# Optimization experiments

Measured on AMD Instinct MI355X. Metric: run time of the kernel, lower is better.

Reference implementation:

```python
import jax, jax.numpy as jnp
import numpy as np

SNUM = 8           # number of select-PUF stages
PUF_LEN = 64       # arbiter PUF length -> phi dim = PUF_LEN + 1
BATCH = 262144     # number of challenge-response pairs
D = 2 ** SNUM      # 256 combinations


def _make_kron_tables():
    """Replicates the W/B kron construction from combineMPUF.__init__.
    Returns Wmat, Bmat of shape [SNUM, D]; row i is W[i]/B[i] (originally [1, D])."""
    tmpX = np.array([[1], [1]])
    Ws, Bs = [], []
    for i in range(SNUM):
        w = np.array([[-1], [1]])
        b = np.array([[1], [0]])
        for _ in range(i + 1, SNUM):
            w = np.kron(tmpX, w)
            b = np.kron(tmpX, b)
        for _ in range(i):
            w = np.kron(w, tmpX)
            b = np.kron(b, tmpX)
        Ws.append(w.T[0])
        Bs.append(b.T[0])
    return (jnp.asarray(np.stack(Ws), jnp.float32),
            jnp.asarray(np.stack(Bs), jnp.float32))


def setup_inputs() -> dict:
    key = jax.random.key(0)
    k_phi, k_ws, k_bs, k_wd, k_bd = jax.random.split(key, 5)
    F = PUF_LEN + 1
    scale = 1.0 / np.sqrt(F)  # ~ torch Linear init scale
    phi = jax.random.normal(k_phi, (BATCH, F), dtype=jnp.float32)
    W_S = jax.random.uniform(k_ws, (SNUM, F), jnp.float32, -scale, scale)
    b_S = jax.random.uniform(k_bs, (SNUM,), jnp.float32, -scale, scale)
    W_D = jax.random.uniform(k_wd, (D, F), jnp.float32, -scale, scale)
    b_D = jax.random.uniform(k_bd, (D,), jnp.float32, -scale, scale)
    Wmat, Bmat = _make_kron_tables()
    return {"phi": phi, "W_S": W_S, "b_S": b_S, "W_D": W_D, "b_D": b_D,
            "Wmat": Wmat, "Bmat": Bmat}


def reference(phi, W_S, b_S, W_D, b_D, Wmat, Bmat):
    # phi: [B, F]; W_S: [SNUM, F]; W_D: [D, F]; Wmat/Bmat: [SNUM, D]
    Sdelta = phi @ W_S.T + b_S            # [B, SNUM]
    Ddelta = phi @ W_D.T + b_D            # [B, D]
    Souts = jax.nn.sigmoid(Sdelta)        # [B, SNUM]
    Douts = jax.nn.sigmoid(Ddelta)        # [B, D]
    # sigmoid-gated outer-product chain: M = prod_i (s_i * w_i + b_i)
    M = jnp.ones_like(Douts)
    for i in range(SNUM):                 # small fixed structural loop
        M = M * (Souts[:, i:i + 1] * Wmat[i] + Bmat[i])
    ans = jnp.sum(Douts * M * 0.99999, axis=-1, keepdims=True)  # [B, 1]
    reliability_output = jnp.abs(Sdelta)  # [B, SNUM]
    return ans, reliability_output
```

## Files before the change

### kernel.cpp

```cpp
#include <hip/hip_runtime.h>

typedef float  f32x4  __attribute__((ext_vector_type(4)));
typedef float  f32x4a __attribute__((ext_vector_type(4), aligned(4)));
typedef float  f32x2a __attribute__((ext_vector_type(2), aligned(4)));
typedef __bf16 bf16x8 __attribute__((ext_vector_type(8)));
typedef short  short8 __attribute__((ext_vector_type(8)));

#define F      65
#define NTT    17
#define KS3    3
#define RPB    128
#define NEGL2E -1.4426950408889634f

__device__ __forceinline__ float fast_sigmoid(float x) {
  float e = __builtin_amdgcn_exp2f(NEGL2E * x);
  return __builtin_amdgcn_rcpf(1.0f + e);
}
__device__ __forceinline__ float sig_prescaled(float a) {
  return __builtin_amdgcn_rcpf(1.0f + __builtin_amdgcn_exp2f(a));
}
template<int CTRL>
__device__ __forceinline__ float dpp_mov(float v) {
  return __builtin_bit_cast(float,
    __builtin_amdgcn_update_dpp(0, __builtin_bit_cast(int, v), CTRL, 0xF, 0xF, true));
}
__device__ __forceinline__ float reduce16(float v) {
  v += dpp_mov<0xB1>(v);
  v += dpp_mov<0x4E>(v);
  v += dpp_mov<0x141>(v);
  v += dpp_mov<0x140>(v);
  return v;
}

__global__ void prep_w(const float* __restrict__ W_S, const float* __restrict__ b_S,
                       const float* __restrict__ W_D, const float* __restrict__ b_D,
                       unsigned short* __restrict__ wsb) {
  int b = blockIdx.x;
  int t = b / 3, s = b % 3;
  int l = threadIdx.x;
  int c = l & 15, q = l >> 4;
  short8 out;
#pragma unroll
  for (int j = 0; j < 8; ++j) {
    int k = 32 * s + 8 * q + j;
    float v = 0.0f;
    if (t < 16) {
      int n = 16 * t + c;
      if (k < F)       v = NEGL2E * W_D[n * F + k];
      else if (k == F) v = NEGL2E * b_D[n];
    } else if (c < 8) {
      if (k < F)       v = W_S[c * F + k];
      else if (k == F) v = b_S[c];
    }
    unsigned int u = __builtin_bit_cast(unsigned int, v);
    u += 0x7FFFu + ((u >> 16) & 1u);
    out[j] = (short)(u >> 16);
  }
  reinterpret_cast<short8*>(wsb)[b * 64 + l] = out;
}

__launch_bounds__(256, 5)
__global__ void mpuf_main(const float* __restrict__ phi,
                          const unsigned short* __restrict__ wsb,
                          float* __restrict__ out_ans,
                          float* __restrict__ out_rel) {
  __shared__ float soutv[RPB][9];
  __shared__ float mtrec[RPB][17];
  __shared__ float mlrec[RPB][17];

  const int tid  = threadIdx.x;
  const int wave = tid >> 6;
  const int l    = tid & 63;
  const int c    = l & 15;
  const int q    = l >> 4;
  const int wrow = wave * 32;
  const int brow = blockIdx.x * RPB;

  const float* prow0 = phi + (size_t)(brow + wrow + c) * F;
  const float* prow1 = prow0 + (size_t)16 * F;

  f32x4a f40[4], f41[4];
#pragma unroll
  for (int s = 0; s < 2; ++s) {
    f40[2 * s]     = *reinterpret_cast<const f32x4a*>(prow0 + 32 * s + 8 * q);
    f40[2 * s + 1] = *reinterpret_cast<const f32x4a*>(prow0 + 32 * s + 8 * q + 4);
    f41[2 * s]     = *reinterpret_cast<const f32x4a*>(prow1 + 32 * s + 8 * q);
    f41[2 * s + 1] = *reinterpret_cast<const f32x4a*>(prow1 + 32 * s + 8 * q + 4);
  }
  const float a640 = prow0[64];
  const float a641 = prow1[64];

  const short8* wsv = reinterpret_cast<const short8*>(wsb);
  short8 bcur[3], bnxt[3];
#pragma unroll
  for (int s = 0; s < 3; ++s) bcur[s] = wsv[(16 * KS3 + s) * 64 + l];
#pragma unroll
  for (int s = 0; s < 3; ++s) bnxt[s] = wsv[s * 64 + l];

  bf16x8 af0[3], af1[3];
#pragma unroll
  for (int s = 0; s < 2; ++s) {
    bf16x8 v0, v1;
#pragma unroll
    for (int j = 0; j < 4; ++j) {
      v0[j]     = (__bf16)f40[2 * s][j];
      v0[j + 4] = (__bf16)f40[2 * s + 1][j];
      v1[j]     = (__bf16)f41[2 * s][j];
      v1[j + 4] = (__bf16)f41[2 * s + 1][j];
    }
    af0[s] = v0; af1[s] = v1;
  }
  {
    bf16x8 v0 = {}, v1 = {};
    if (q == 0) {
      v0[0] = (__bf16)a640; v0[1] = (__bf16)1.0f;
      v1[0] = (__bf16)a641; v1[1] = (__bf16)1.0f;
    }
    af0[2] = v0; af1[2] = v1;
  }

  f32x4 aS0 = {}, aS1 = {};
#pragma unroll
  for (int s = 0; s < KS3; ++s) {
    bf16x8 b = __builtin_bit_cast(bf16x8, bcur[s]);
    aS0 = __builtin_amdgcn_mfma_f32_16x16x32_bf16(af0[s], b, aS0, 0, 0, 0);
    aS1 = __builtin_amdgcn_mfma_f32_16x16x32_bf16(af1[s], b, aS1, 0, 0, 0);
  }
  if (c < 8) {
#pragma unroll
    for (int r = 0; r < 4; ++r) {
      const int R0 = wrow + q * 4 + r, R1 = R0 + 16;
      out_rel[(size_t)(brow + R0) * 8 + c] = fabsf(aS0[r]);
      out_rel[(size_t)(brow + R1) * 8 + c] = fabsf(aS1[r]);
      soutv[R0][c] = fast_sigmoid(aS0[r]);
      soutv[R1][c] = fast_sigmoid(aS1[r]);
    }
  }

#pragma unroll
  for (int rr = 0; rr < 8; ++rr) {
    const int R = wrow + (rr & 4) * 4 + q * 4 + (rr & 3);
    f32x2a p01 = *reinterpret_cast<const f32x2a*>(&soutv[R][0]);
    f32x2a p23 = *reinterpret_cast<const f32x2a*>(&soutv[R][2]);
    f32x2a p45 = *reinterpret_cast<const f32x2a*>(&soutv[R][4]);
    f32x2a p67 = *reinterpret_cast<const f32x2a*>(&soutv[R][6]);
    float m = 0.99999f;
    m *= (c & 1) ? p01[0] : 1.0f - p01[0];
    m *= (c & 2) ? p01[1] : 1.0f - p01[1];
    m *= (c & 4) ? p23[0] : 1.0f - p23[0];
    m *= (c & 8) ? p23[1] : 1.0f - p23[1];
    mlrec[R][c] = m;
    float mt = (c & 1) ? p45[0] : 1.0f - p45[0];
    mt *= (c & 2) ? p45[1] : 1.0f - p45[1];
    mt *= (c & 4) ? p67[0] : 1.0f - p67[0];
    mt *= (c & 8) ? p67[1] : 1.0f - p67[1];
    mtrec[R][c] = mt;
  }

  float ans0[4] = {0, 0, 0, 0}, ans1[4] = {0, 0, 0, 0};

#pragma unroll 1
  for (int t = 0; t < 16; ++t) {
    f32x4 A0 = {}, A1 = {};
#pragma unroll
    for (int s = 0; s < KS3; ++s) {
      bf16x8 b = __builtin_bit_cast(bf16x8, bnxt[s]);
      A0 = __builtin_amdgcn_mfma_f32_16x16x32_bf16(af0[s], b, A0, 0, 0, 0);
      A1 = __builtin_amdgcn_mfma_f32_16x16x32_bf16(af1[s], b, A1, 0, 0, 0);
    }
    const int tn = (t < 15) ? t + 1 : 15;
#pragma unroll
    for (int s = 0; s < 3; ++s) bnxt[s] = wsv[(tn * KS3 + s) * 64 + l];
#pragma unroll
    for (int r = 0; r < 4; ++r) {
      const int R0 = wrow + q * 4 + r, R1 = R0 + 16;
      float w0 = mtrec[R0][t];
      float w1 = mtrec[R1][t];
      ans0[r] = fmaf(sig_prescaled(A0[r]), w0, ans0[r]);
      ans1[r] = fmaf(sig_prescaled(A1[r]), w1, ans1[r]);
    }
  }

#pragma unroll
  for (int r = 0; r < 4; ++r) {
    const int R0 = wrow + q * 4 + r, R1 = R0 + 16;
    ans0[r] = reduce16(mlrec[R0][c] * ans0[r]);
    ans1[r] = reduce16(mlrec[R1][c] * ans1[r]);
  }
  if (c == 0) {
    f32x4 o0 = { ans0[0], ans0[1], ans0[2], ans0[3] };
    f32x4 o1 = { ans1[0], ans1[1], ans1[2], ans1[3] };
    *reinterpret_cast<f32x4*>(&out_ans[brow + wrow + q * 4])      = o0;
    *reinterpret_cast<f32x4*>(&out_ans[brow + wrow + 16 + q * 4]) = o1;
  }
}

extern "C" void kernel_launch(void* const* d_in, const int* in_sizes, int n_in,
                              void* d_out, int out_size, void* d_ws, size_t ws_size,
                              hipStream_t stream) {
  const float* phi = (const float*)d_in[0];
  const float* W_S = (const float*)d_in[1];
  const float* b_S = (const float*)d_in[2];
  const float* W_D = (const float*)d_in[3];
  const float* b_D = (const float*)d_in[4];
  const int rows = in_sizes[0] / F;
  unsigned short* wsb = (unsigned short*)d_ws;
  float* out_ans = (float*)d_out;
  float* out_rel = out_ans + rows;
  hipLaunchKernelGGL(prep_w, dim3(NTT * KS3), dim3(64), 0, stream,
                     W_S, b_S, W_D, b_D, wsb);
  hipLaunchKernelGGL(mpuf_main, dim3(rows / RPB), dim3(256), 0, stream,
                     phi, wsb, out_ans, out_rel);
}
```

Before: 41.24 us.

## Stage phi through padded LDS with coalesced loads; keep ml products in registers

Each wave now loads its contiguous 32-row phi slab with fully coalesced 16-byte global loads, scatters it into a padded LDS buffer, then reads per-lane row fragments from LDS to build the bf16 MFMA operands. Before, each lane made strided unaligned row loads. The mlrec shared array is replaced by per-lane registers, since each lane already computes the values it later consumes. The new slab buffer adds about 35 KB of LDS per block, and launch bounds drop from 5 to 4 blocks per CU, which lowers occupancy.

```diff
diff --git a/kernel.cpp b/kernel.cpp
--- a/kernel.cpp
+++ b/kernel.cpp
@@ -1,7 +1,6 @@
 #include <hip/hip_runtime.h>
 
 typedef float  f32x4  __attribute__((ext_vector_type(4)));
-typedef float  f32x4a __attribute__((ext_vector_type(4), aligned(4)));
 typedef float  f32x2a __attribute__((ext_vector_type(2), aligned(4)));
 typedef __bf16 bf16x8 __attribute__((ext_vector_type(8)));
 typedef short  short8 __attribute__((ext_vector_type(8)));
@@ -10,6 +9,8 @@
 #define NTT    17
 #define KS3    3
 #define RPB    128
+#define PADROW 68
+#define SLABDW (32 * PADROW)
 #define NEGL2E -1.4426950408889634f
 
 __device__ __forceinline__ float fast_sigmoid(float x) {
@@ -59,14 +60,14 @@
   reinterpret_cast<short8*>(wsb)[b * 64 + l] = out;
 }
 
-__launch_bounds__(256, 5)
+__launch_bounds__(256, 4)
 __global__ void mpuf_main(const float* __restrict__ phi,
                           const unsigned short* __restrict__ wsb,
                           float* __restrict__ out_ans,
                           float* __restrict__ out_rel) {
+  __shared__ __align__(16) float ldsPhi[4 * SLABDW];
   __shared__ float soutv[RPB][9];
   __shared__ float mtrec[RPB][17];
-  __shared__ float mlrec[RPB][17];
 
   const int tid  = threadIdx.x;
   const int wave = tid >> 6;
@@ -76,19 +77,13 @@
   const int wrow = wave * 32;
   const int brow = blockIdx.x * RPB;
 
-  const float* prow0 = phi + (size_t)(brow + wrow + c) * F;
-  const float* prow1 = prow0 + (size_t)16 * F;
-
-  f32x4a f40[4], f41[4];
-#pragma unroll
-  for (int s = 0; s < 2; ++s) {
-    f40[2 * s]     = *reinterpret_cast<const f32x4a*>(prow0 + 32 * s + 8 * q);
-    f40[2 * s + 1] = *reinterpret_cast<const f32x4a*>(prow0 + 32 * s + 8 * q + 4);
-    f41[2 * s]     = *reinterpret_cast<const f32x4a*>(prow1 + 32 * s + 8 * q);
-    f41[2 * s + 1] = *reinterpret_cast<const f32x4a*>(prow1 + 32 * s + 8 * q + 4);
-  }
-  const float a640 = prow0[64];
-  const float a641 = prow1[64];
+  const float* slab = phi + (size_t)(brow + wrow) * F;
+  f32x4 st[9];
+#pragma unroll
+  for (int i = 0; i < 9; ++i) {
+    if (i < 8 || l < 8)
+      st[i] = *reinterpret_cast<const f32x4*>(slab + 4 * (l + 64 * i));
+  }
 
   const short8* wsv = reinterpret_cast<const short8*>(wsb);
   short8 bcur[3], bnxt[3];
@@ -97,26 +92,38 @@
 #pragma unroll
   for (int s = 0; s < 3; ++s) bnxt[s] = wsv[s * 64 + l];
 
+  float* myslab = &ldsPhi[wave * SLABDW];
+#pragma unroll
+  for (int i = 0; i < 9; ++i) {
+    if (i < 8 || l < 8) {
+#pragma unroll
+      for (int j = 0; j < 4; ++j) {
+        int gi = 4 * (l + 64 * i) + j;
+        myslab[gi + 3 * (gi / 65)] = st[i][j];
+      }
+    }
+  }
+
   bf16x8 af0[3], af1[3];
 #pragma unroll
-  for (int s = 0; s < 2; ++s) {
-    bf16x8 v0, v1;
-#pragma unroll
-    for (int j = 0; j < 4; ++j) {
-      v0[j]     = (__bf16)f40[2 * s][j];
-      v0[j + 4] = (__bf16)f40[2 * s + 1][j];
-      v1[j]     = (__bf16)f41[2 * s][j];
-      v1[j + 4] = (__bf16)f41[2 * s + 1][j];
-    }
-    af0[s] = v0; af1[s] = v1;
-  }
-  {
-    bf16x8 v0 = {}, v1 = {};
-    if (q == 0) {
-      v0[0] = (__bf16)a640; v0[1] = (__bf16)1.0f;
-      v1[0] = (__bf16)a641; v1[1] = (__bf16)1.0f;
-    }
-    af0[2] = v0; af1[2] = v1;
+  for (int h = 0; h < 2; ++h) {
+    bf16x8* af = h ? af1 : af0;
+    const float* rb = &myslab[PADROW * (c + 16 * h)];
+#pragma unroll
+    for (int s = 0; s < 2; ++s) {
+      f32x4 lo = *reinterpret_cast<const f32x4*>(rb + 32 * s + 8 * q);
+      f32x4 hi = *reinterpret_cast<const f32x4*>(rb + 32 * s + 8 * q + 4);
+      bf16x8 v;
+#pragma unroll
+      for (int j = 0; j < 4; ++j) {
+        v[j]     = (__bf16)lo[j];
+        v[j + 4] = (__bf16)hi[j];
+      }
+      af[s] = v;
+    }
+    bf16x8 v = {};
+    if (q == 0) { v[0] = (__bf16)rb[64]; v[1] = (__bf16)1.0f; }
+    af[2] = v;
   }
 
   f32x4 aS0 = {}, aS1 = {};
@@ -137,6 +144,7 @@
     }
   }
 
+  float Ml0[4], Ml1[4];
 #pragma unroll
   for (int rr = 0; rr < 8; ++rr) {
     const int R = wrow + (rr & 4) * 4 + q * 4 + (rr & 3);
@@ -149,7 +157,7 @@
     m *= (c & 2) ? p01[1] : 1.0f - p01[1];
     m *= (c & 4) ? p23[0] : 1.0f - p23[0];
     m *= (c & 8) ? p23[1] : 1.0f - p23[1];
-    mlrec[R][c] = m;
+    if (rr < 4) Ml0[rr & 3] = m; else Ml1[rr & 3] = m;
     float mt = (c & 1) ? p45[0] : 1.0f - p45[0];
     mt *= (c & 2) ? p45[1] : 1.0f - p45[1];
     mt *= (c & 4) ? p67[0] : 1.0f - p67[0];
@@ -183,9 +191,8 @@
 
 #pragma unroll
   for (int r = 0; r < 4; ++r) {
-    const int R0 = wrow + q * 4 + r, R1 = R0 + 16;
-    ans0[r] = reduce16(mlrec[R0][c] * ans0[r]);
-    ans1[r] = reduce16(mlrec[R1][c] * ans1[r]);
+    ans0[r] = reduce16(Ml0[r] * ans0[r]);
+    ans1[r] = reduce16(Ml1[r] * ans1[r]);
   }
   if (c == 0) {
     f32x4 o0 = { ans0[0], ans0[1], ans0[2], ans0[3] };
```

New measurement: 43.68 us. 5.9% more time.

## Stage packed weights in LDS and fully unroll the tile loop

Applied to the files above, without the earlier changes.

Each block now copies the whole packed bf16 weight buffer (about 52 KB) into shared memory once and reads B fragments from LDS, where before every wave streamed them from global memory with a one-tile prefetch. The tile loop is fully unrolled, the mtrec weights are read as float4 vectors, and the mlrec products stay in registers instead of LDS. The large LDS footprint lowers the launch-bounds occupancy target from 5 to 2 blocks per CU and adds a block-wide barrier, so latency hiding may suffer. Every block also repeats the full weight copy.

```diff
diff --git a/kernel.cpp b/kernel.cpp
--- a/kernel.cpp
+++ b/kernel.cpp
@@ -10,6 +10,7 @@
 #define NTT    17
 #define KS3    3
 #define RPB    128
+#define NCHUNK (NTT*KS3*64)
 #define NEGL2E -1.4426950408889634f
 
 __device__ __forceinline__ float fast_sigmoid(float x) {
@@ -59,14 +60,14 @@
   reinterpret_cast<short8*>(wsb)[b * 64 + l] = out;
 }
 
-__launch_bounds__(256, 5)
+__launch_bounds__(256, 2)
 __global__ void mpuf_main(const float* __restrict__ phi,
                           const unsigned short* __restrict__ wsb,
                           float* __restrict__ out_ans,
                           float* __restrict__ out_rel) {
-  __shared__ float soutv[RPB][9];
-  __shared__ float mtrec[RPB][17];
-  __shared__ float mlrec[RPB][17];
+  __shared__ short8 ldsB[NCHUNK];
+  __shared__ float  soutv[RPB][9];
+  __shared__ float  mtrec[RPB][20];
 
   const int tid  = threadIdx.x;
   const int wave = tid >> 6;
@@ -91,11 +92,11 @@
   const float a641 = prow1[64];
 
   const short8* wsv = reinterpret_cast<const short8*>(wsb);
-  short8 bcur[3], bnxt[3];
-#pragma unroll
-  for (int s = 0; s < 3; ++s) bcur[s] = wsv[(16 * KS3 + s) * 64 + l];
-#pragma unroll
-  for (int s = 0; s < 3; ++s) bnxt[s] = wsv[s * 64 + l];
+#pragma unroll
+  for (int i = 0; i < 13; ++i) {
+    int idx = tid + i * 256;
+    if (idx < NCHUNK) ldsB[idx] = wsv[idx];
+  }
 
   bf16x8 af0[3], af1[3];
 #pragma unroll
@@ -103,10 +104,10 @@
     bf16x8 v0, v1;
 #pragma unroll
     for (int j = 0; j < 4; ++j) {
-      v0[j]     = (__bf16)f40[2 * s][j];
-      v0[j + 4] = (__bf16)f40[2 * s + 1][j];
-      v1[j]     = (__bf16)f41[2 * s][j];
-      v1[j + 4] = (__bf16)f41[2 * s + 1][j];
+      v0[j]     = (__bf16)f40[s * 2][j];
+      v0[j + 4] = (__bf16)f40[s * 2 + 1][j];
+      v1[j]     = (__bf16)f41[s * 2][j];
+      v1[j + 4] = (__bf16)f41[s * 2 + 1][j];
     }
     af0[s] = v0; af1[s] = v1;
   }
@@ -119,10 +120,12 @@
     af0[2] = v0; af1[2] = v1;
   }
 
+  __syncthreads();
+
   f32x4 aS0 = {}, aS1 = {};
 #pragma unroll
   for (int s = 0; s < KS3; ++s) {
-    bf16x8 b = __builtin_bit_cast(bf16x8, bcur[s]);
+    bf16x8 b = __builtin_bit_cast(bf16x8, ldsB[(16 * KS3 + s) * 64 + l]);
     aS0 = __builtin_amdgcn_mfma_f32_16x16x32_bf16(af0[s], b, aS0, 0, 0, 0);
     aS1 = __builtin_amdgcn_mfma_f32_16x16x32_bf16(af1[s], b, aS1, 0, 0, 0);
   }
@@ -137,6 +140,7 @@
     }
   }
 
+  float Ml0[4], Ml1[4];
 #pragma unroll
   for (int rr = 0; rr < 8; ++rr) {
     const int R = wrow + (rr & 4) * 4 + q * 4 + (rr & 3);
@@ -149,7 +153,7 @@
     m *= (c & 2) ? p01[1] : 1.0f - p01[1];
     m *= (c & 4) ? p23[0] : 1.0f - p23[0];
     m *= (c & 8) ? p23[1] : 1.0f - p23[1];
-    mlrec[R][c] = m;
+    if (rr < 4) Ml0[rr & 3] = m; else Ml1[rr & 3] = m;
     float mt = (c & 1) ? p45[0] : 1.0f - p45[0];
     mt *= (c & 2) ? p45[1] : 1.0f - p45[1];
     mt *= (c & 4) ? p67[0] : 1.0f - p67[0];
@@ -159,33 +163,37 @@
 
   float ans0[4] = {0, 0, 0, 0}, ans1[4] = {0, 0, 0, 0};
 
-#pragma unroll 1
-  for (int t = 0; t < 16; ++t) {
-    f32x4 A0 = {}, A1 = {};
-#pragma unroll
-    for (int s = 0; s < KS3; ++s) {
-      bf16x8 b = __builtin_bit_cast(bf16x8, bnxt[s]);
-      A0 = __builtin_amdgcn_mfma_f32_16x16x32_bf16(af0[s], b, A0, 0, 0, 0);
-      A1 = __builtin_amdgcn_mfma_f32_16x16x32_bf16(af1[s], b, A1, 0, 0, 0);
-    }
-    const int tn = (t < 15) ? t + 1 : 15;
-#pragma unroll
-    for (int s = 0; s < 3; ++s) bnxt[s] = wsv[(tn * KS3 + s) * 64 + l];
+#pragma unroll
+  for (int tp = 0; tp < 4; ++tp) {
+    f32x4 w0[4], w1[4];
 #pragma unroll
     for (int r = 0; r < 4; ++r) {
-      const int R0 = wrow + q * 4 + r, R1 = R0 + 16;
-      float w0 = mtrec[R0][t];
-      float w1 = mtrec[R1][t];
-      ans0[r] = fmaf(sig_prescaled(A0[r]), w0, ans0[r]);
-      ans1[r] = fmaf(sig_prescaled(A1[r]), w1, ans1[r]);
+      const int R0 = wrow + q * 4 + r;
+      w0[r] = *reinterpret_cast<const f32x4*>(&mtrec[R0][4 * tp]);
+      w1[r] = *reinterpret_cast<const f32x4*>(&mtrec[R0 + 16][4 * tp]);
+    }
+#pragma unroll
+    for (int tt = 0; tt < 4; ++tt) {
+      const int t = 4 * tp + tt;
+      f32x4 A0 = {}, A1 = {};
+#pragma unroll
+      for (int s = 0; s < KS3; ++s) {
+        bf16x8 b = __builtin_bit_cast(bf16x8, ldsB[(t * KS3 + s) * 64 + l]);
+        A0 = __builtin_amdgcn_mfma_f32_16x16x32_bf16(af0[s], b, A0, 0, 0, 0);
+        A1 = __builtin_amdgcn_mfma_f32_16x16x32_bf16(af1[s], b, A1, 0, 0, 0);
+      }
+#pragma unroll
+      for (int r = 0; r < 4; ++r) {
+        ans0[r] = fmaf(sig_prescaled(A0[r]), w0[r][tt], ans0[r]);
+        ans1[r] = fmaf(sig_prescaled(A1[r]), w1[r][tt], ans1[r]);
+      }
     }
   }
 
 #pragma unroll
   for (int r = 0; r < 4; ++r) {
-    const int R0 = wrow + q * 4 + r, R1 = R0 + 16;
-    ans0[r] = reduce16(mlrec[R0][c] * ans0[r]);
-    ans1[r] = reduce16(mlrec[R1][c] * ans1[r]);
+    ans0[r] = reduce16(Ml0[r] * ans0[r]);
+    ans1[r] = reduce16(Ml1[r] * ans1[r]);
   }
   if (c == 0) {
     f32x4 o0 = { ans0[0], ans0[1], ans0[2], ans0[3] };
```

Measured after the change: 44.78 us. 1.09x slower.

## Coalesce reliability stores via LDS, keep Ml in registers, stagger weight tile order

Applied to the files above, without the earlier changes.

The reliability outputs are staged through a shared-memory tile and written as float4 per row instead of scattered scalar stores. The low-half mask products now stay in registers instead of an LDS array, which frees shared memory, and the launch bound is raised to 6 blocks per CU. Each block starts its 16-tile weight loop at a block-dependent offset so concurrent blocks read different weight tiles, and the next-tile prefetch is issued before the MFMAs. The trade-off is extra register pressure from Ml0/Ml1 and the higher occupancy target, which may cause spills.

```diff
diff --git a/kernel.cpp b/kernel.cpp
--- a/kernel.cpp
+++ b/kernel.cpp
@@ -59,14 +59,14 @@
   reinterpret_cast<short8*>(wsb)[b * 64 + l] = out;
 }
 
-__launch_bounds__(256, 5)
+__launch_bounds__(256, 6)
 __global__ void mpuf_main(const float* __restrict__ phi,
                           const unsigned short* __restrict__ wsb,
                           float* __restrict__ out_ans,
                           float* __restrict__ out_rel) {
-  __shared__ float soutv[RPB][9];
+  __shared__ float soutv[RPB][10];
   __shared__ float mtrec[RPB][17];
-  __shared__ float mlrec[RPB][17];
+  __shared__ float relv[RPB][8];
 
   const int tid  = threadIdx.x;
   const int wave = tid >> 6;
@@ -75,6 +75,7 @@
   const int q    = l >> 4;
   const int wrow = wave * 32;
   const int brow = blockIdx.x * RPB;
+  const int tbase = blockIdx.x & 15;
 
   const float* prow0 = phi + (size_t)(brow + wrow + c) * F;
   const float* prow1 = prow0 + (size_t)16 * F;
@@ -91,11 +92,11 @@
   const float a641 = prow1[64];
 
   const short8* wsv = reinterpret_cast<const short8*>(wsb);
-  short8 bcur[3], bnxt[3];
-#pragma unroll
-  for (int s = 0; s < 3; ++s) bcur[s] = wsv[(16 * KS3 + s) * 64 + l];
-#pragma unroll
-  for (int s = 0; s < 3; ++s) bnxt[s] = wsv[s * 64 + l];
+  short8 bS[3], bnxt[3];
+#pragma unroll
+  for (int s = 0; s < 3; ++s) bS[s]   = wsv[(16 * KS3 + s) * 64 + l];
+#pragma unroll
+  for (int s = 0; s < 3; ++s) bnxt[s] = wsv[(tbase * KS3 + s) * 64 + l];
 
   bf16x8 af0[3], af1[3];
 #pragma unroll
@@ -103,10 +104,10 @@
     bf16x8 v0, v1;
 #pragma unroll
     for (int j = 0; j < 4; ++j) {
-      v0[j]     = (__bf16)f40[2 * s][j];
-      v0[j + 4] = (__bf16)f40[2 * s + 1][j];
-      v1[j]     = (__bf16)f41[2 * s][j];
-      v1[j + 4] = (__bf16)f41[2 * s + 1][j];
+      v0[j]     = (__bf16)f40[s * 2][j];
+      v0[j + 4] = (__bf16)f40[s * 2 + 1][j];
+      v1[j]     = (__bf16)f41[s * 2][j];
+      v1[j + 4] = (__bf16)f41[s * 2 + 1][j];
     }
     af0[s] = v0; af1[s] = v1;
   }
@@ -122,7 +123,7 @@
   f32x4 aS0 = {}, aS1 = {};
 #pragma unroll
   for (int s = 0; s < KS3; ++s) {
-    bf16x8 b = __builtin_bit_cast(bf16x8, bcur[s]);
+    bf16x8 b = __builtin_bit_cast(bf16x8, bS[s]);
     aS0 = __builtin_amdgcn_mfma_f32_16x16x32_bf16(af0[s], b, aS0, 0, 0, 0);
     aS1 = __builtin_amdgcn_mfma_f32_16x16x32_bf16(af1[s], b, aS1, 0, 0, 0);
   }
@@ -130,13 +131,21 @@
 #pragma unroll
     for (int r = 0; r < 4; ++r) {
       const int R0 = wrow + q * 4 + r, R1 = R0 + 16;
-      out_rel[(size_t)(brow + R0) * 8 + c] = fabsf(aS0[r]);
-      out_rel[(size_t)(brow + R1) * 8 + c] = fabsf(aS1[r]);
+      relv[R0][c] = fabsf(aS0[r]);
+      relv[R1][c] = fabsf(aS1[r]);
       soutv[R0][c] = fast_sigmoid(aS0[r]);
       soutv[R1][c] = fast_sigmoid(aS1[r]);
     }
   }
 
+  {
+    const int row = l >> 1, half = l & 1;
+    f32x4 v = *reinterpret_cast<const f32x4*>(&relv[wrow + row][half * 4]);
+    *reinterpret_cast<f32x4*>(
+        &out_rel[(size_t)(brow + wrow + row) * 8 + half * 4]) = v;
+  }
+
+  float Ml0[4], Ml1[4];
 #pragma unroll
   for (int rr = 0; rr < 8; ++rr) {
     const int R = wrow + (rr & 4) * 4 + q * 4 + (rr & 3);
@@ -149,7 +158,7 @@
     m *= (c & 2) ? p01[1] : 1.0f - p01[1];
     m *= (c & 4) ? p23[0] : 1.0f - p23[0];
     m *= (c & 8) ? p23[1] : 1.0f - p23[1];
-    mlrec[R][c] = m;
+    if (rr < 4) Ml0[rr & 3] = m; else Ml1[rr & 3] = m;
     float mt = (c & 1) ? p45[0] : 1.0f - p45[0];
     mt *= (c & 2) ? p45[1] : 1.0f - p45[1];
     mt *= (c & 4) ? p67[0] : 1.0f - p67[0];
@@ -160,17 +169,22 @@
   float ans0[4] = {0, 0, 0, 0}, ans1[4] = {0, 0, 0, 0};
 
 #pragma unroll 1
-  for (int t = 0; t < 16; ++t) {
+  for (int tt = 0; tt < 16; ++tt) {
+    const int t  = (tt + tbase) & 15;
+    const int tn = (tt + 1 + tbase) & 15;
+    short8 bt[3];
+#pragma unroll
+    for (int s = 0; s < 3; ++s) bt[s] = bnxt[s];
+#pragma unroll
+    for (int s = 0; s < 3; ++s)
+      bnxt[s] = wsv[(tn * KS3 + s) * 64 + l];
     f32x4 A0 = {}, A1 = {};
 #pragma unroll
     for (int s = 0; s < KS3; ++s) {
-      bf16x8 b = __builtin_bit_cast(bf16x8, bnxt[s]);
+      bf16x8 b = __builtin_bit_cast(bf16x8, bt[s]);
       A0 = __builtin_amdgcn_mfma_f32_16x16x32_bf16(af0[s], b, A0, 0, 0, 0);
       A1 = __builtin_amdgcn_mfma_f32_16x16x32_bf16(af1[s], b, A1, 0, 0, 0);
     }
-    const int tn = (t < 15) ? t + 1 : 15;
-#pragma unroll
-    for (int s = 0; s < 3; ++s) bnxt[s] = wsv[(tn * KS3 + s) * 64 + l];
 #pragma unroll
     for (int r = 0; r < 4; ++r) {
       const int R0 = wrow + q * 4 + r, R1 = R0 + 16;
@@ -181,15 +195,13 @@
     }
   }
 
+  f32x4 o0, o1;
 #pragma unroll
   for (int r = 0; r < 4; ++r) {
-    const int R0 = wrow + q * 4 + r, R1 = R0 + 16;
-    ans0[r] = reduce16(mlrec[R0][c] * ans0[r]);
-    ans1[r] = reduce16(mlrec[R1][c] * ans1[r]);
+    o0[r] = reduce16(Ml0[r] * ans0[r]);
+    o1[r] = reduce16(Ml1[r] * ans1[r]);
   }
   if (c == 0) {
-    f32x4 o0 = { ans0[0], ans0[1], ans0[2], ans0[3] };
-    f32x4 o1 = { ans1[0], ans1[1], ans1[2], ans1[3] };
     *reinterpret_cast<f32x4*>(&out_ans[brow + wrow + q * 4])      = o0;
     *reinterpret_cast<f32x4*>(&out_ans[brow + wrow + 16 + q * 4]) = o1;
   }
```

New measurement: 47.87 us. 16.1% more time.
